# Performance work log

Hardware: AMD Instinct MI355X
Metric: run time of the kernel (lower is better)

The kernel has to match this reference:

```python
import jax, jax.numpy as jnp
import numpy as np

DN = ('NCHW', 'OIHW', 'NCHW')

def _conv(x, W, pad):
    return jax.lax.conv_general_dilated(x, W, (1, 1), [(pad, pad), (pad, pad)], dimension_numbers=DN)

def _cbs(x, W, s, b, pad):
    # Conv2d(bias=False) + folded BatchNorm (scale/bias) + SiLU
    y = _conv(x, W, pad) * s[None, :, None, None] + b[None, :, None, None]
    return y * jax.nn.sigmoid(y)

def _l2norm(x):
    n = jnp.sqrt(jnp.sum(x * x, axis=1, keepdims=True))
    return x / jnp.maximum(n, 1e-12)

def setup_inputs() -> dict:
    key = jax.random.key(0)
    ks = jax.random.split(key, 24)
    B, C, H, L, TD, NC = 16, 256, 64, 40, 768, 8
    EMB = (TD + NC * 2) // 2  # 392
    w = lambda k, sh: jax.random.normal(k, sh, jnp.float32) * 0.02
    img = jax.random.normal(ks[0], (B, C, H, H), jnp.float32)
    flang = jax.random.normal(ks[1], (B, L, TD), jnp.float32)
    lengths = jax.random.randint(ks[2], (B, 1), 5, L + 1)
    word_mask = (jnp.arange(L)[None, :] < lengths).astype(jnp.int32)
    return {
        'img': img, 'flang': flang, 'word_mask': word_mask, 'sigma_w': 0.1,
        'W1': w(ks[3], (EMB, TD)), 'b1': w(ks[4], (EMB,)),
        'W2': w(ks[5], (NC * 2, EMB)), 'b2': w(ks[6], (NC * 2,)),
        'Wv': w(ks[7], (C, C, 1, 1)), 'sv': jnp.ones((C,)), 'bv': w(ks[8], (C,)),
        'Wg': w(ks[9], (NC, NC, 1, 1)), 'sg': jnp.ones((NC,)), 'bg': w(ks[10], (NC,)),
        'Wb': w(ks[11], (NC, NC, 1, 1)), 'sb': jnp.ones((NC,)), 'bb': w(ks[12], (NC,)),
        'Wf1': w(ks[13], (C, C, 1, 1)), 'sf1': jnp.ones((C,)), 'bf1': w(ks[14], (C,)),
        'Wf2': w(ks[15], (C, C, 3, 3)), 'sf2': jnp.ones((C,)), 'bf2': w(ks[16], (C,)),
        'Wf3': w(ks[17], (C, C, 1, 1)), 'bf3': w(ks[18], (C,)),
        'Ws': w(ks[19], (NC, C, 3, 3)), 'bs': w(ks[20], (NC,)),
        'add_weight': jnp.zeros((), jnp.float32),
    }

def reference(img, flang, word_mask, sigma_w, W1, b1, W2, b2, Wv, sv, bv,
              Wg, sg, bg, Wb, sb, bb, Wf1, sf1, bf1, Wf2, sf2, bf2,
              Wf3, bf3, Ws, bs, add_weight):
    B, C, H = img.shape[0], img.shape[1], img.shape[2]
    nc = Wg.shape[0]
    map_visu = jnp.tanh(_cbs(img, Wv, sv, bv, 0))
    # ragged masked mean excluding first (CLS) and last (SEP) masked tokens
    m = word_mask.astype(jnp.float32)
    c = jnp.cumsum(m, axis=1)
    tot = c[:, -1:]
    inc = m * ((c > 1) & (c < tot)).astype(jnp.float32)  # [B,L]
    flang_avg = jnp.sum(flang * inc[:, :, None], axis=1) / jnp.sum(inc, axis=1, keepdims=True)
    map_flang = jax.nn.sigmoid((flang_avg @ W1.T + b1) @ W2.T + b2)  # [B,2*nc]
    maps = map_flang.reshape(B, nc, 2)
    sigma_x = sigma_w * H
    sig = _conv(img, Ws, 0) + bs[None, :, None, None]  # [B,nc,H-2,H-2]
    sigma_weight = jax.nn.sigmoid(jnp.mean(sig, axis=(2, 3), keepdims=True))  # [B,nc,1,1]
    sigma_y = sigma_x * sigma_weight
    yc = (maps[:, :, 0] * H).astype(jnp.int32).astype(jnp.float32)[:, :, None, None]
    xc = (maps[:, :, 1] * H).astype(jnp.int32).astype(jnp.float32)[:, :, None, None]
    gy = jnp.arange(H, dtype=jnp.float32)[None, None, :, None]
    gx = jnp.arange(H, dtype=jnp.float32)[None, None, None, :]
    weights = jnp.exp(-((gy - yc) ** 2 / (2.0 * sigma_y ** 2) + (gx - xc) ** 2 / (2.0 * sigma_x ** 2)))  # [B,nc,H,H]
    gamma = jnp.tanh(_cbs(weights, Wg, sg, bg, 0))
    beta = jnp.tanh(_cbs(weights, Wb, sb, bb, 0))
    g = jnp.mean(gamma, axis=1, keepdims=True)
    bmax = jnp.max(beta, axis=1, keepdims=True)
    v_film = _l2norm(g * map_visu + bmax)
    v_film = _cbs(v_film, Wf1, sf1, bf1, 0)
    v_film = _cbs(v_film, Wf2, sf2, bf2, 1)
    v_film = _conv(v_film, Wf3, 0) + bf3[None, :, None, None]
    aw = jnp.tanh(add_weight)
    v_add = (1.0 + aw) * img + (1.0 - aw) * v_film
    return _l2norm(v_add)
```

## Files before the change

kernel.cpp:

```cpp
#include <hip/hip_runtime.h>
#include <hip/hip_bf16.h>


#define DEVFN static __device__ __forceinline__

DEVFN float sigmoidf_(float x) { return 1.f / (1.f + expf(-x)); }
DEVFN float siluf_(float y) { return y / (1.f + expf(-y)); }

typedef __attribute__((ext_vector_type(8))) short bf16x8;
typedef __attribute__((ext_vector_type(4))) float f32x4;

DEVFN unsigned short f2bf_(float f) {
    union { __hip_bfloat16 b; unsigned short u; } cv;
    cv.b = __float2bfloat16(f);
    return cv.u;
}

__global__ void prep_kernel(const float* __restrict__ Wv, const float* __restrict__ Wf1,
                            const float* __restrict__ Wf3, const float* __restrict__ Wf2,
                            short* __restrict__ WvB, short* __restrict__ W1B,
                            short* __restrict__ W3B, short* __restrict__ WB2) {
    int idx = blockIdx.x * 256 + threadIdx.x;
    if (idx < 65536) {
        int j    = idx & 7;
        int lane = (idx >> 3) & 63;
        int coT  = (idx >> 9) & 15;
        int ci32 = (idx >> 13) & 7;
        int co = coT * 16 + (lane & 15);
        int ci = ci32 * 32 + ((lane >> 4) << 3) + j;
        int src = co * 256 + ci;
        WvB[idx] = (short)f2bf_(Wv[src]);
        W1B[idx] = (short)f2bf_(Wf1[src]);
        W3B[idx] = (short)f2bf_(Wf3[src]);
    }
    int o = idx - 65536;
    if (o >= 0 && o < 589824) {
        int j    = o & 7;
        int lane = (o >> 3) & 63;
        int coT  = (o >> 9) & 15;
        int ci32 = (o >> 13) & 7;
        int kk   = o >> 16;
        int co = coT * 16 + (lane & 15);
        int ci = ci32 * 32 + ((lane >> 4) << 3) + j;
        WB2[o] = (short)f2bf_(Wf2[(co * 256 + ci) * 9 + kk]);
    }
}

__global__ void lang_kernel(const float* __restrict__ flang, const int* __restrict__ mask,
                            float* __restrict__ fa) {
    __shared__ float inc[40];
    __shared__ float isum;
    int b = blockIdx.x, t = threadIdx.x;
    if (t == 0) {
        float cum[40];
        float c = 0.f;
        for (int l = 0; l < 40; ++l) { c += (float)mask[b * 40 + l]; cum[l] = c; }
        float tot = c, s = 0.f;
        for (int l = 0; l < 40; ++l) {
            float m = (float)mask[b * 40 + l];
            float v = (cum[l] > 1.f && cum[l] < tot) ? m : 0.f;
            inc[l] = v; s += v;
        }
        isum = s;
    }
    __syncthreads();
    for (int d = t; d < 768; d += 256) {
        float a = 0.f;
        for (int l = 0; l < 40; ++l) a += flang[(size_t)(b * 40 + l) * 768 + d] * inc[l];
        fa[b * 768 + d] = a / isum;
    }
}

__global__ void mlp_kernel(const float* __restrict__ fa_g, const float* __restrict__ W1,
                           const float* __restrict__ b1, const float* __restrict__ W2,
                           const float* __restrict__ b2, float* __restrict__ ycxc) {
    __shared__ float fa[768];
    __shared__ float h[392];
    __shared__ float o[16];
    int b = blockIdx.x, t = threadIdx.x;
    for (int k = t; k < 768; k += 448) fa[k] = fa_g[b * 768 + k];
    __syncthreads();
    if (t < 392) {
        float a = b1[t];
        const float* w = W1 + (size_t)t * 768;
        for (int k = 0; k < 768; ++k) a = fmaf(fa[k], w[k], a);
        h[t] = a;
    }
    __syncthreads();
    if (t < 16) {
        float a = b2[t];
        const float* w = W2 + (size_t)t * 392;
        for (int k = 0; k < 392; ++k) a = fmaf(h[k], w[k], a);
        o[t] = sigmoidf_(a);
    }
    __syncthreads();
    if (t < 8) {
        ycxc[b * 8 + t]       = (float)(int)(o[2 * t] * 64.f);
        ycxc[128 + b * 8 + t] = (float)(int)(o[2 * t + 1] * 64.f);
    }
}

__global__ void wsum_kernel(const float* __restrict__ img, float* __restrict__ S) {
    __shared__ float red[9 * 256];
    int bc = blockIdx.x;
    int t = threadIdx.x;
    float s[9];
#pragma unroll
    for (int k = 0; k < 9; ++k) s[k] = 0.f;
    const float* p = img + (size_t)bc * 4096;
    for (int j = 0; j < 16; ++j) {
        int idx = t + j * 256;
        int y = idx >> 6, x = idx & 63;
        float v = p[idx];
#pragma unroll
        for (int ky = 0; ky < 3; ++ky) {
            if (y < ky || y > ky + 61) continue;
#pragma unroll
            for (int kx = 0; kx < 3; ++kx) {
                if (x < kx || x > kx + 61) continue;
                s[ky * 3 + kx] += v;
            }
        }
    }
#pragma unroll
    for (int k = 0; k < 9; ++k) red[k * 256 + t] = s[k];
    __syncthreads();
    for (int st = 128; st > 0; st >>= 1) {
        if (t < st) {
#pragma unroll
            for (int k = 0; k < 9; ++k) red[k * 256 + t] += red[k * 256 + t + st];
        }
        __syncthreads();
    }
    if (t < 9) S[(size_t)bc * 9 + t] = red[t * 256];
}

__global__ void sigw_kernel(const float* __restrict__ Ws, const float* __restrict__ S,
                            const float* __restrict__ bs, float* __restrict__ sigw) {
    __shared__ float red[8 * 256];
    int b = blockIdx.x, t = threadIdx.x;
    float sv[9];
    const float* Sp = S + (size_t)(b * 256 + t) * 9;
#pragma unroll
    for (int k = 0; k < 9; ++k) sv[k] = Sp[k];
#pragma unroll
    for (int co = 0; co < 8; ++co) {
        const float* wp = Ws + (size_t)(co * 256 + t) * 9;
        float a = 0.f;
#pragma unroll
        for (int k = 0; k < 9; ++k) a = fmaf(wp[k], sv[k], a);
        red[co * 256 + t] = a;
    }
    __syncthreads();
    for (int st = 128; st > 0; st >>= 1) {
        if (t < st) {
#pragma unroll
            for (int co = 0; co < 8; ++co) red[co * 256 + t] += red[co * 256 + t + st];
        }
        __syncthreads();
    }
    if (t < 8) sigw[b * 8 + t] = sigmoidf_(red[t * 256] / 3844.f + bs[t]);
}

__global__ void gauss_kernel(const float* __restrict__ ycxc, const float* __restrict__ sigw,
                             const float* __restrict__ sigma_w,
                             const float* __restrict__ Wg, const float* __restrict__ sg,
                             const float* __restrict__ bg,
                             const float* __restrict__ Wb, const float* __restrict__ sb,
                             const float* __restrict__ bb,
                             float* __restrict__ g, float* __restrict__ bm) {
    int blk = blockIdx.x;
    int b = blk >> 6, y = blk & 63;
    int x = threadIdx.x;
    float sx = sigma_w[0] * 64.f;
    float w[8];
#pragma unroll
    for (int n = 0; n < 8; ++n) {
        float yc = ycxc[b * 8 + n], xc = ycxc[128 + b * 8 + n];
        float sy = sx * sigw[b * 8 + n];
        float dy = (float)y - yc, dx = (float)x - xc;
        w[n] = expf(-(dy * dy / (2.f * sy * sy) + dx * dx / (2.f * sx * sx)));
    }
    float gacc = 0.f, bmax = -3.4e38f;
#pragma unroll
    for (int n = 0; n < 8; ++n) {
        float a1 = 0.f, a2 = 0.f;
#pragma unroll
        for (int m = 0; m < 8; ++m) {
            a1 = fmaf(Wg[n * 8 + m], w[m], a1);
            a2 = fmaf(Wb[n * 8 + m], w[m], a2);
        }
        float ga = tanhf(siluf_(a1 * sg[n] + bg[n]));
        float be = tanhf(siluf_(a2 * sb[n] + bb[n]));
        gacc += ga;
        bmax = fmaxf(bmax, be);
    }
    g[(size_t)(b * 64 + y) * 64 + x] = gacc * 0.125f;
    bm[(size_t)(b * 64 + y) * 64 + x] = bmax;
}

template <int MODE>
__global__ __launch_bounds__(256) void mfma1x1(
        const float* __restrict__ inF,
        const __hip_bfloat16* __restrict__ inB,
        const short* __restrict__ wb,
        const float* __restrict__ sc, const float* __restrict__ bi,
        const float* __restrict__ g, const float* __restrict__ bm,
        const float* __restrict__ img, const float* __restrict__ addw,
        __hip_bfloat16* __restrict__ outB, float* __restrict__ outF) {
    __shared__ __attribute__((aligned(16))) short lA[64 * 264];
    __shared__ float ls_s[256], ls_b[256];
    __shared__ float ls_g[64], ls_bm[64];
    int blk = blockIdx.x, b = blk >> 6, y = blk & 63;
    int t = threadIdx.x, w = t >> 6, lane = t & 63;
    int lx = lane & 15, koct = lane >> 4;

    if (MODE != 2) { ls_s[t] = sc[t]; }
    ls_b[t] = bi[t];
    if (MODE == 0 && t < 64) {
        ls_g[t]  = g[(size_t)(b * 64 + y) * 64 + t];
        ls_bm[t] = bm[(size_t)(b * 64 + y) * 64 + t];
    }

    if (MODE == 0) {
        int x = t & 63, cg = t >> 6;
        const float* ib = inF + (size_t)b * 1048576 + y * 64 + x;
#pragma unroll
        for (int c8 = 0; c8 < 8; ++c8) {
            int ci0 = cg * 64 + c8 * 8;
            unsigned short r[8];
#pragma unroll
            for (int j = 0; j < 8; ++j) r[j] = f2bf_(ib[(size_t)(ci0 + j) * 4096]);
            *(uint4*)&lA[x * 264 + ci0] = *(uint4*)r;
        }
    } else {
        const unsigned short* xg = (const unsigned short*)inB + (size_t)(b * 64 + y) * 16384;
#pragma unroll
        for (int it = 0; it < 8; ++it) {
            int e8 = t + it * 256;
            int x2 = e8 >> 5, c8 = e8 & 31;
            *(uint4*)&lA[x2 * 264 + c8 * 8] = *(const uint4*)(xg + e8 * 8);
        }
    }

    f32x4 acc[4][4];
#pragma unroll
    for (int mi = 0; mi < 4; ++mi)
#pragma unroll
        for (int ni = 0; ni < 4; ++ni) acc[mi][ni] = (f32x4){0.f, 0.f, 0.f, 0.f};
    __syncthreads();

#pragma unroll
    for (int k32 = 0; k32 < 8; ++k32) {
        const short* wp = wb + (((k32 * 16) + w * 4) * 64 + lane) * 8;
        bf16x8 bfr[4];
#pragma unroll
        for (int ni = 0; ni < 4; ++ni) bfr[ni] = *(const bf16x8*)(wp + ni * 512);
        bf16x8 afr[4];
#pragma unroll
        for (int mi = 0; mi < 4; ++mi)
            afr[mi] = *(const bf16x8*)&lA[(mi * 16 + lx) * 264 + k32 * 32 + koct * 8];
#pragma unroll
        for (int mi = 0; mi < 4; ++mi)
#pragma unroll
            for (int ni = 0; ni < 4; ++ni)
                acc[mi][ni] = __builtin_amdgcn_mfma_f32_16x16x32_bf16(afr[mi], bfr[ni], acc[mi][ni], 0, 0, 0);
    }

    if constexpr (MODE == 0) {
        __shared__ float pr[4096];
        __shared__ float invs[64];
#pragma unroll
        for (int mi = 0; mi < 4; ++mi)
#pragma unroll
            for (int rr = 0; rr < 4; ++rr) {
                int x = mi * 16 + koct * 4 + rr;
                float ps = 0.f;
#pragma unroll
                for (int ni = 0; ni < 4; ++ni) {
                    int co = w * 64 + ni * 16 + lx;
                    float yv = fmaf(acc[mi][ni][rr], ls_s[co], ls_b[co]);
                    float mvv = tanhf(siluf_(yv));
                    float v = fmaf(ls_g[x], mvv, ls_bm[x]);
                    acc[mi][ni][rr] = v;
                    ps += v * v;
                }
                pr[x * 64 + w * 16 + lx] = ps;
            }
        __syncthreads();
        if (t < 64) {
            float s2 = 0.f;
            for (int q = 0; q < 64; ++q) s2 += pr[t * 64 + q];
            invs[t] = 1.f / fmaxf(sqrtf(s2), 1e-12f);
        }
        __syncthreads();
#pragma unroll
        for (int mi = 0; mi < 4; ++mi)
#pragma unroll
            for (int ni = 0; ni < 4; ++ni) {
                int co = w * 64 + ni * 16 + lx;
#pragma unroll
                for (int rr = 0; rr < 4; ++rr) {
                    int x = mi * 16 + koct * 4 + rr;
                    lA[x * 264 + co] = (short)f2bf_(acc[mi][ni][rr] * invs[x]);
                }
            }
        __syncthreads();
        unsigned short* og = (unsigned short*)outB + (size_t)(b * 64 + y) * 16384;
#pragma unroll
        for (int it = 0; it < 8; ++it) {
            int e8 = t + it * 256;
            int x2 = e8 >> 5, c8 = e8 & 31;
            *(uint4*)(og + e8 * 8) = *(uint4*)&lA[x2 * 264 + c8 * 8];
        }
    } else if constexpr (MODE == 1) {
        __syncthreads();
#pragma unroll
        for (int mi = 0; mi < 4; ++mi)
#pragma unroll
            for (int ni = 0; ni < 4; ++ni) {
                int co = w * 64 + ni * 16 + lx;
#pragma unroll
                for (int rr = 0; rr < 4; ++rr) {
                    int x = mi * 16 + koct * 4 + rr;
                    float yv = fmaf(acc[mi][ni][rr], ls_s[co], ls_b[co]);
                    lA[x * 264 + co] = (short)f2bf_(siluf_(yv));
                }
            }
        __syncthreads();
        unsigned short* og = (unsigned short*)outB + (size_t)(b * 64 + y) * 16384;
#pragma unroll
        for (int it = 0; it < 8; ++it) {
            int e8 = t + it * 256;
            int x2 = e8 >> 5, c8 = e8 & 31;
            *(uint4*)(og + e8 * 8) = *(uint4*)&lA[x2 * 264 + c8 * 8];
        }
    } else {
        __shared__ float pr[4096];
        __shared__ float invs[64];
        float aw = tanhf(addw[0]);
#pragma unroll
        for (int mi = 0; mi < 4; ++mi)
#pragma unroll
            for (int ni = 0; ni < 4; ++ni) {
                int co = w * 64 + ni * 16 + lx;
                const float* ip = img + ((size_t)(b * 256 + co) * 64 + y) * 64 + mi * 16 + koct * 4;
                float4 im = *(const float4*)ip;
                float imv[4] = {im.x, im.y, im.z, im.w};
#pragma unroll
                for (int rr = 0; rr < 4; ++rr) {
                    float v = (1.f + aw) * imv[rr] + (1.f - aw) * (acc[mi][ni][rr] + ls_b[co]);
                    acc[mi][ni][rr] = v;
                }
            }
#pragma unroll
        for (int mi = 0; mi < 4; ++mi)
#pragma unroll
            for (int rr = 0; rr < 4; ++rr) {
                int x = mi * 16 + koct * 4 + rr;
                float ps = 0.f;
#pragma unroll
                for (int ni = 0; ni < 4; ++ni) ps += acc[mi][ni][rr] * acc[mi][ni][rr];
                pr[x * 64 + w * 16 + lx] = ps;
            }
        __syncthreads();
        if (t < 64) {
            float s2 = 0.f;
            for (int q = 0; q < 64; ++q) s2 += pr[t * 64 + q];
            invs[t] = 1.f / fmaxf(sqrtf(s2), 1e-12f);
        }
        __syncthreads();
#pragma unroll
        for (int mi = 0; mi < 4; ++mi)
#pragma unroll
            for (int ni = 0; ni < 4; ++ni) {
                int co = w * 64 + ni * 16 + lx;
                float r[4];
#pragma unroll
                for (int rr = 0; rr < 4; ++rr) {
                    int x = mi * 16 + koct * 4 + rr;
                    r[rr] = acc[mi][ni][rr] * invs[x];
                }
                float* op = outF + ((size_t)(b * 256 + co) * 64 + y) * 64 + mi * 16 + koct * 4;
                *(float4*)op = *(float4*)r;
            }
    }
}

__global__ __launch_bounds__(256, 3) void conv3x3_mfma(const __hip_bfloat16* __restrict__ xin,
                                                       const short* __restrict__ wb,
                                                       const float* __restrict__ sc,
                                                       const float* __restrict__ bi,
                                                       __hip_bfloat16* __restrict__ outB) {
    __shared__ __attribute__((aligned(16))) short lds[64 * 264];
    int blk = blockIdx.x;
    int b = blk >> 6, y = blk & 63;
    int t = threadIdx.x;
    int w = t >> 6, lane = t & 63;
    int lx = lane & 15, koct = lane >> 4;
    const unsigned short* xg = (const unsigned short*)xin + (size_t)b * 1048576;

    f32x4 acc[4][4];
#pragma unroll
    for (int mi = 0; mi < 4; ++mi)
#pragma unroll
        for (int ni = 0; ni < 4; ++ni) acc[mi][ni] = (f32x4){0.f, 0.f, 0.f, 0.f};

    for (int cc = 0; cc < 4; ++cc) {
        __syncthreads();
#pragma unroll
        for (int p = 0; p < 7; ++p) {
            int u = t + p * 256;
            if (u < 1584) {
                int r = u / 528;
                int rem = u - r * 528;
                int xp = rem >> 3, ci8 = rem & 7;
                int ys = y + r - 1, xs = xp - 1;
                uint4 v = {0u, 0u, 0u, 0u};
                if (ys >= 0 && ys < 64 && xs >= 0 && xs < 64)
                    v = *(const uint4*)(xg + ((size_t)(ys * 64 + xs) * 256 + cc * 64 + ci8 * 8));
                *(uint4*)&lds[(r * 66 + xp) * 72 + ci8 * 8] = v;
            }
        }
        __syncthreads();
        for (int kk = 0; kk < 9; ++kk) {
            int ky = kk / 3, kx = kk - ky * 3;
#pragma unroll
            for (int k32 = 0; k32 < 2; ++k32) {
                int ci32g = cc * 2 + k32;
                const short* wp = wb + ((((kk * 8 + ci32g) * 16) + w * 4) * 64 + lane) * 8;
                bf16x8 bfr[4];
#pragma unroll
                for (int ni = 0; ni < 4; ++ni)
                    bfr[ni] = *(const bf16x8*)(wp + ni * 512);
                bf16x8 afr[4];
#pragma unroll
                for (int mi = 0; mi < 4; ++mi)
                    afr[mi] = *(const bf16x8*)&lds[(ky * 66 + mi * 16 + lx + kx) * 72 + k32 * 32 + koct * 8];
#pragma unroll
                for (int mi = 0; mi < 4; ++mi)
#pragma unroll
                    for (int ni = 0; ni < 4; ++ni)
                        acc[mi][ni] = __builtin_amdgcn_mfma_f32_16x16x32_bf16(afr[mi], bfr[ni], acc[mi][ni], 0, 0, 0);
            }
        }
    }
    __syncthreads();
#pragma unroll
    for (int ni = 0; ni < 4; ++ni) {
        int co = w * 64 + ni * 16 + lx;
        float s = sc[co], bb2 = bi[co];
#pragma unroll
        for (int mi = 0; mi < 4; ++mi)
#pragma unroll
            for (int rr = 0; rr < 4; ++rr) {
                int x = mi * 16 + koct * 4 + rr;
                float yv = fmaf(acc[mi][ni][rr], s, bb2);
                lds[x * 264 + co] = (short)f2bf_(siluf_(yv));
            }
    }
    __syncthreads();
    unsigned short* og = (unsigned short*)outB + (size_t)(b * 64 + y) * 16384;
#pragma unroll
    for (int it = 0; it < 8; ++it) {
        int e8 = t + it * 256;
        int x2 = e8 >> 5, c8 = e8 & 31;
        *(uint4*)(og + e8 * 8) = *(uint4*)&lds[x2 * 264 + c8 * 8];
    }
}

extern "C" void kernel_launch(void* const* d_in, const int* in_sizes, int n_in,
                              void* d_out, int out_size, void* d_ws, size_t ws_size,
                              hipStream_t stream) {
    const float* img     = (const float*)d_in[0];
    const float* flang   = (const float*)d_in[1];
    const int*   wmask   = (const int*)d_in[2];
    const float* sigma_w = (const float*)d_in[3];
    const float* W1      = (const float*)d_in[4];
    const float* b1      = (const float*)d_in[5];
    const float* W2      = (const float*)d_in[6];
    const float* b2      = (const float*)d_in[7];
    const float* Wv      = (const float*)d_in[8];
    const float* sv      = (const float*)d_in[9];
    const float* bv      = (const float*)d_in[10];
    const float* Wg      = (const float*)d_in[11];
    const float* sg      = (const float*)d_in[12];
    const float* bg      = (const float*)d_in[13];
    const float* Wb      = (const float*)d_in[14];
    const float* sb      = (const float*)d_in[15];
    const float* bb      = (const float*)d_in[16];
    const float* Wf1     = (const float*)d_in[17];
    const float* sf1     = (const float*)d_in[18];
    const float* bf1     = (const float*)d_in[19];
    const float* Wf2     = (const float*)d_in[20];
    const float* sf2     = (const float*)d_in[21];
    const float* bf2     = (const float*)d_in[22];
    const float* Wf3     = (const float*)d_in[23];
    const float* bf3     = (const float*)d_in[24];
    const float* Ws      = (const float*)d_in[25];
    const float* bs      = (const float*)d_in[26];
    const float* addw    = (const float*)d_in[27];
    float* out = (float*)d_out;
    float* ws  = (float*)d_ws;

    short* WvB  = (short*)ws;
    short* W1B  = (short*)(ws + 32768);
    short* W3B  = (short*)(ws + 65536);
    short* WB2  = (short*)(ws + 98304);
    float* fa   = ws + 393216;
    float* ycxc = ws + 405504;
    float* S    = ws + 405760;
    float* sigw = ws + 442624;
    float* gmap = ws + 442752;
    float* bmap = ws + 508288;
    __hip_bfloat16* bufA = (__hip_bfloat16*)(ws + 573824);
    __hip_bfloat16* bufB = (__hip_bfloat16*)(ws + 8962432);

    prep_kernel<<<2560, 256, 0, stream>>>(Wv, Wf1, Wf3, Wf2, WvB, W1B, W3B, WB2);
    lang_kernel<<<16, 256, 0, stream>>>(flang, wmask, fa);
    mlp_kernel<<<16, 448, 0, stream>>>(fa, W1, b1, W2, b2, ycxc);
    wsum_kernel<<<4096, 256, 0, stream>>>(img, S);
    sigw_kernel<<<16, 256, 0, stream>>>(Ws, S, bs, sigw);
    gauss_kernel<<<1024, 64, 0, stream>>>(ycxc, sigw, sigma_w, Wg, sg, bg, Wb, sb, bb, gmap, bmap);
    mfma1x1<0><<<1024, 256, 0, stream>>>(img, nullptr, WvB, sv, bv, gmap, bmap,
                                         nullptr, nullptr, bufA, nullptr);
    mfma1x1<1><<<1024, 256, 0, stream>>>(nullptr, bufA, W1B, sf1, bf1, nullptr, nullptr,
                                         nullptr, nullptr, bufB, nullptr);
    conv3x3_mfma<<<1024, 256, 0, stream>>>(bufB, WB2, sf2, bf2, bufA);
    mfma1x1<2><<<1024, 256, 0, stream>>>(nullptr, bufA, W3B, nullptr, bf3, nullptr, nullptr,
                                         img, addw, nullptr, out);
}
```

Before: 465.7 us.

## Fuse Wv and Wf1 1x1 convs; process two rows per 3x3 conv block

Merges the first two 1x1 MFMA convolutions into one kernel, so the normalized FiLM activations stay in LDS and are never written to or re-read from global memory. The 3x3 conv now computes two output rows per block with a 4-row halo tile. This reuses the halo loads and weight fragments across both rows, at the cost of doubling accumulator registers (occupancy hint lowered to 2). The final 1x1 conv is split into its own kernel, and the pr scratch array is aliased onto LDS to reduce shared memory use.

```diff
diff --git a/kernel.cpp b/kernel.cpp
--- a/kernel.cpp
+++ b/kernel.cpp
@@ -199,32 +199,32 @@
     bm[(size_t)(b * 64 + y) * 64 + x] = bmax;
 }
 
-template <int MODE>
-__global__ __launch_bounds__(256) void mfma1x1(
-        const float* __restrict__ inF,
-        const __hip_bfloat16* __restrict__ inB,
-        const short* __restrict__ wb,
-        const float* __restrict__ sc, const float* __restrict__ bi,
+__global__ __launch_bounds__(256) void f01_kernel(
+        const float* __restrict__ img, const short* __restrict__ wvb,
+        const short* __restrict__ w1b,
+        const float* __restrict__ sv, const float* __restrict__ bv,
+        const float* __restrict__ s1, const float* __restrict__ b1,
         const float* __restrict__ g, const float* __restrict__ bm,
-        const float* __restrict__ img, const float* __restrict__ addw,
-        __hip_bfloat16* __restrict__ outB, float* __restrict__ outF) {
+        __hip_bfloat16* __restrict__ outB) {
     __shared__ __attribute__((aligned(16))) short lA[64 * 264];
-    __shared__ float ls_s[256], ls_b[256];
+    __shared__ float invs[64];
+    __shared__ float ls_sv[256], ls_bv[256], ls_s1[256], ls_b1[256];
     __shared__ float ls_g[64], ls_bm[64];
+    float* pr = (float*)lA;
     int blk = blockIdx.x, b = blk >> 6, y = blk & 63;
     int t = threadIdx.x, w = t >> 6, lane = t & 63;
     int lx = lane & 15, koct = lane >> 4;
 
-    if (MODE != 2) { ls_s[t] = sc[t]; }
-    ls_b[t] = bi[t];
-    if (MODE == 0 && t < 64) {
+    ls_sv[t] = sv[t]; ls_bv[t] = bv[t];
+    ls_s1[t] = s1[t]; ls_b1[t] = b1[t];
+    if (t < 64) {
         ls_g[t]  = g[(size_t)(b * 64 + y) * 64 + t];
         ls_bm[t] = bm[(size_t)(b * 64 + y) * 64 + t];
     }
 
-    if (MODE == 0) {
+    {
         int x = t & 63, cg = t >> 6;
-        const float* ib = inF + (size_t)b * 1048576 + y * 64 + x;
+        const float* ib = img + (size_t)b * 1048576 + y * 64 + x;
 #pragma unroll
         for (int c8 = 0; c8 < 8; ++c8) {
             int ci0 = cg * 64 + c8 * 8;
@@ -233,16 +233,7 @@
             for (int j = 0; j < 8; ++j) r[j] = f2bf_(ib[(size_t)(ci0 + j) * 4096]);
             *(uint4*)&lA[x * 264 + ci0] = *(uint4*)r;
         }
-    } else {
-        const unsigned short* xg = (const unsigned short*)inB + (size_t)(b * 64 + y) * 16384;
-#pragma unroll
-        for (int it = 0; it < 8; ++it) {
-            int e8 = t + it * 256;
-            int x2 = e8 >> 5, c8 = e8 & 31;
-            *(uint4*)&lA[x2 * 264 + c8 * 8] = *(const uint4*)(xg + e8 * 8);
-        }
-    }
-
+    }
     f32x4 acc[4][4];
 #pragma unroll
     for (int mi = 0; mi < 4; ++mi)
@@ -252,7 +243,7 @@
 
 #pragma unroll
     for (int k32 = 0; k32 < 8; ++k32) {
-        const short* wp = wb + (((k32 * 16) + w * 4) * 64 + lane) * 8;
+        const short* wp = wvb + (((k32 * 16) + w * 4) * 64 + lane) * 8;
         bf16x8 bfr[4];
 #pragma unroll
         for (int ni = 0; ni < 4; ++ni) bfr[ni] = *(const bf16x8*)(wp + ni * 512);
@@ -266,156 +257,119 @@
             for (int ni = 0; ni < 4; ++ni)
                 acc[mi][ni] = __builtin_amdgcn_mfma_f32_16x16x32_bf16(afr[mi], bfr[ni], acc[mi][ni], 0, 0, 0);
     }
-
-    if constexpr (MODE == 0) {
-        __shared__ float pr[4096];
-        __shared__ float invs[64];
-#pragma unroll
-        for (int mi = 0; mi < 4; ++mi)
+    __syncthreads();
+
+#pragma unroll
+    for (int mi = 0; mi < 4; ++mi)
+#pragma unroll
+        for (int rr = 0; rr < 4; ++rr) {
+            int x = mi * 16 + koct * 4 + rr;
+            float ps = 0.f;
+#pragma unroll
+            for (int ni = 0; ni < 4; ++ni) {
+                int co = w * 64 + ni * 16 + lx;
+                float yv = fmaf(acc[mi][ni][rr], ls_sv[co], ls_bv[co]);
+                float mvv = tanhf(siluf_(yv));
+                float v = fmaf(ls_g[x], mvv, ls_bm[x]);
+                acc[mi][ni][rr] = v;
+                ps += v * v;
+            }
+            pr[x * 64 + w * 16 + lx] = ps;
+        }
+    __syncthreads();
+    if (t < 64) {
+        float s2 = 0.f;
+        for (int q = 0; q < 64; ++q) s2 += pr[t * 64 + q];
+        invs[t] = 1.f / fmaxf(sqrtf(s2), 1e-12f);
+    }
+    __syncthreads();
+
+#pragma unroll
+    for (int mi = 0; mi < 4; ++mi)
+#pragma unroll
+        for (int ni = 0; ni < 4; ++ni) {
+            int co = w * 64 + ni * 16 + lx;
 #pragma unroll
             for (int rr = 0; rr < 4; ++rr) {
                 int x = mi * 16 + koct * 4 + rr;
-                float ps = 0.f;
-#pragma unroll
-                for (int ni = 0; ni < 4; ++ni) {
-                    int co = w * 64 + ni * 16 + lx;
-                    float yv = fmaf(acc[mi][ni][rr], ls_s[co], ls_b[co]);
-                    float mvv = tanhf(siluf_(yv));
-                    float v = fmaf(ls_g[x], mvv, ls_bm[x]);
-                    acc[mi][ni][rr] = v;
-                    ps += v * v;
-                }
-                pr[x * 64 + w * 16 + lx] = ps;
-            }
-        __syncthreads();
-        if (t < 64) {
-            float s2 = 0.f;
-            for (int q = 0; q < 64; ++q) s2 += pr[t * 64 + q];
-            invs[t] = 1.f / fmaxf(sqrtf(s2), 1e-12f);
-        }
-        __syncthreads();
+                lA[x * 264 + co] = (short)f2bf_(acc[mi][ni][rr] * invs[x]);
+            }
+        }
+#pragma unroll
+    for (int mi = 0; mi < 4; ++mi)
+#pragma unroll
+        for (int ni = 0; ni < 4; ++ni) acc[mi][ni] = (f32x4){0.f, 0.f, 0.f, 0.f};
+    __syncthreads();
+
+#pragma unroll
+    for (int k32 = 0; k32 < 8; ++k32) {
+        const short* wp = w1b + (((k32 * 16) + w * 4) * 64 + lane) * 8;
+        bf16x8 bfr[4];
+#pragma unroll
+        for (int ni = 0; ni < 4; ++ni) bfr[ni] = *(const bf16x8*)(wp + ni * 512);
+        bf16x8 afr[4];
 #pragma unroll
         for (int mi = 0; mi < 4; ++mi)
-#pragma unroll
-            for (int ni = 0; ni < 4; ++ni) {
-                int co = w * 64 + ni * 16 + lx;
-#pragma unroll
-                for (int rr = 0; rr < 4; ++rr) {
-                    int x = mi * 16 + koct * 4 + rr;
-                    lA[x * 264 + co] = (short)f2bf_(acc[mi][ni][rr] * invs[x]);
-                }
-            }
-        __syncthreads();
-        unsigned short* og = (unsigned short*)outB + (size_t)(b * 64 + y) * 16384;
-#pragma unroll
-        for (int it = 0; it < 8; ++it) {
-            int e8 = t + it * 256;
-            int x2 = e8 >> 5, c8 = e8 & 31;
-            *(uint4*)(og + e8 * 8) = *(uint4*)&lA[x2 * 264 + c8 * 8];
-        }
-    } else if constexpr (MODE == 1) {
-        __syncthreads();
+            afr[mi] = *(const bf16x8*)&lA[(mi * 16 + lx) * 264 + k32 * 32 + koct * 8];
 #pragma unroll
         for (int mi = 0; mi < 4; ++mi)
 #pragma unroll
-            for (int ni = 0; ni < 4; ++ni) {
-                int co = w * 64 + ni * 16 + lx;
-#pragma unroll
-                for (int rr = 0; rr < 4; ++rr) {
-                    int x = mi * 16 + koct * 4 + rr;
-                    float yv = fmaf(acc[mi][ni][rr], ls_s[co], ls_b[co]);
-                    lA[x * 264 + co] = (short)f2bf_(siluf_(yv));
-                }
-            }
-        __syncthreads();
-        unsigned short* og = (unsigned short*)outB + (size_t)(b * 64 + y) * 16384;
-#pragma unroll
-        for (int it = 0; it < 8; ++it) {
-            int e8 = t + it * 256;
-            int x2 = e8 >> 5, c8 = e8 & 31;
-            *(uint4*)(og + e8 * 8) = *(uint4*)&lA[x2 * 264 + c8 * 8];
-        }
-    } else {
-        __shared__ float pr[4096];
-        __shared__ float invs[64];
-        float aw = tanhf(addw[0]);
-#pragma unroll
-        for (int mi = 0; mi < 4; ++mi)
-#pragma unroll
-            for (int ni = 0; ni < 4; ++ni) {
-                int co = w * 64 + ni * 16 + lx;
-                const float* ip = img + ((size_t)(b * 256 + co) * 64 + y) * 64 + mi * 16 + koct * 4;
-                float4 im = *(const float4*)ip;
-                float imv[4] = {im.x, im.y, im.z, im.w};
-#pragma unroll
-                for (int rr = 0; rr < 4; ++rr) {
-                    float v = (1.f + aw) * imv[rr] + (1.f - aw) * (acc[mi][ni][rr] + ls_b[co]);
-                    acc[mi][ni][rr] = v;
-                }
-            }
-#pragma unroll
-        for (int mi = 0; mi < 4; ++mi)
+            for (int ni = 0; ni < 4; ++ni)
+                acc[mi][ni] = __builtin_amdgcn_mfma_f32_16x16x32_bf16(afr[mi], bfr[ni], acc[mi][ni], 0, 0, 0);
+    }
+    __syncthreads();
+
+#pragma unroll
+    for (int mi = 0; mi < 4; ++mi)
+#pragma unroll
+        for (int ni = 0; ni < 4; ++ni) {
+            int co = w * 64 + ni * 16 + lx;
 #pragma unroll
             for (int rr = 0; rr < 4; ++rr) {
                 int x = mi * 16 + koct * 4 + rr;
-                float ps = 0.f;
-#pragma unroll
-                for (int ni = 0; ni < 4; ++ni) ps += acc[mi][ni][rr] * acc[mi][ni][rr];
-                pr[x * 64 + w * 16 + lx] = ps;
-            }
-        __syncthreads();
-        if (t < 64) {
-            float s2 = 0.f;
-            for (int q = 0; q < 64; ++q) s2 += pr[t * 64 + q];
-            invs[t] = 1.f / fmaxf(sqrtf(s2), 1e-12f);
-        }
-        __syncthreads();
-#pragma unroll
-        for (int mi = 0; mi < 4; ++mi)
-#pragma unroll
-            for (int ni = 0; ni < 4; ++ni) {
-                int co = w * 64 + ni * 16 + lx;
-                float r[4];
-#pragma unroll
-                for (int rr = 0; rr < 4; ++rr) {
-                    int x = mi * 16 + koct * 4 + rr;
-                    r[rr] = acc[mi][ni][rr] * invs[x];
-                }
-                float* op = outF + ((size_t)(b * 256 + co) * 64 + y) * 64 + mi * 16 + koct * 4;
-                *(float4*)op = *(float4*)r;
-            }
-    }
-}
-
-__global__ __launch_bounds__(256, 3) void conv3x3_mfma(const __hip_bfloat16* __restrict__ xin,
+                float yv = fmaf(acc[mi][ni][rr], ls_s1[co], ls_b1[co]);
+                lA[x * 264 + co] = (short)f2bf_(siluf_(yv));
+            }
+        }
+    __syncthreads();
+    unsigned short* og = (unsigned short*)outB + (size_t)(b * 64 + y) * 16384;
+#pragma unroll
+    for (int it = 0; it < 8; ++it) {
+        int e8 = t + it * 256;
+        int x2 = e8 >> 5, c8 = e8 & 31;
+        *(uint4*)(og + e8 * 8) = *(uint4*)&lA[x2 * 264 + c8 * 8];
+    }
+}
+
+__global__ __launch_bounds__(256, 2) void conv3x3_mfma(const __hip_bfloat16* __restrict__ xin,
                                                        const short* __restrict__ wb,
                                                        const float* __restrict__ sc,
                                                        const float* __restrict__ bi,
                                                        __hip_bfloat16* __restrict__ outB) {
-    __shared__ __attribute__((aligned(16))) short lds[64 * 264];
+    __shared__ __attribute__((aligned(16))) short lds[4 * 66 * 72];
     int blk = blockIdx.x;
-    int b = blk >> 6, y = blk & 63;
+    int b = blk >> 5, y0 = (blk & 31) * 2;
     int t = threadIdx.x;
     int w = t >> 6, lane = t & 63;
     int lx = lane & 15, koct = lane >> 4;
     const unsigned short* xg = (const unsigned short*)xin + (size_t)b * 1048576;
 
-    f32x4 acc[4][4];
-#pragma unroll
-    for (int mi = 0; mi < 4; ++mi)
+    f32x4 acc[8][4];
+#pragma unroll
+    for (int mi = 0; mi < 8; ++mi)
 #pragma unroll
         for (int ni = 0; ni < 4; ++ni) acc[mi][ni] = (f32x4){0.f, 0.f, 0.f, 0.f};
 
     for (int cc = 0; cc < 4; ++cc) {
         __syncthreads();
 #pragma unroll
-        for (int p = 0; p < 7; ++p) {
+        for (int p = 0; p < 9; ++p) {
             int u = t + p * 256;
-            if (u < 1584) {
+            if (u < 2112) {
                 int r = u / 528;
                 int rem = u - r * 528;
                 int xp = rem >> 3, ci8 = rem & 7;
-                int ys = y + r - 1, xs = xp - 1;
+                int ys = y0 + r - 1, xs = xp - 1;
                 uint4 v = {0u, 0u, 0u, 0u};
                 if (ys >= 0 && ys < 64 && xs >= 0 && xs < 64)
                     v = *(const uint4*)(xg + ((size_t)(ys * 64 + xs) * 256 + cc * 64 + ci8 * 8));
@@ -433,40 +387,142 @@
 #pragma unroll
                 for (int ni = 0; ni < 4; ++ni)
                     bfr[ni] = *(const bf16x8*)(wp + ni * 512);
-                bf16x8 afr[4];
-#pragma unroll
-                for (int mi = 0; mi < 4; ++mi)
-                    afr[mi] = *(const bf16x8*)&lds[(ky * 66 + mi * 16 + lx + kx) * 72 + k32 * 32 + koct * 8];
-#pragma unroll
-                for (int mi = 0; mi < 4; ++mi)
+                bf16x8 afr[8];
+#pragma unroll
+                for (int mi = 0; mi < 8; ++mi) {
+                    int row = mi >> 2, xb = (mi & 3) * 16;
+                    afr[mi] = *(const bf16x8*)&lds[((row + ky) * 66 + xb + lx + kx) * 72 + k32 * 32 + koct * 8];
+                }
+#pragma unroll
+                for (int mi = 0; mi < 8; ++mi)
 #pragma unroll
                     for (int ni = 0; ni < 4; ++ni)
                         acc[mi][ni] = __builtin_amdgcn_mfma_f32_16x16x32_bf16(afr[mi], bfr[ni], acc[mi][ni], 0, 0, 0);
             }
         }
     }
-    __syncthreads();
-#pragma unroll
-    for (int ni = 0; ni < 4; ++ni) {
-        int co = w * 64 + ni * 16 + lx;
-        float s = sc[co], bb2 = bi[co];
-#pragma unroll
-        for (int mi = 0; mi < 4; ++mi)
-#pragma unroll
-            for (int rr = 0; rr < 4; ++rr) {
-                int x = mi * 16 + koct * 4 + rr;
-                float yv = fmaf(acc[mi][ni][rr], s, bb2);
-                lds[x * 264 + co] = (short)f2bf_(siluf_(yv));
-            }
-    }
-    __syncthreads();
-    unsigned short* og = (unsigned short*)outB + (size_t)(b * 64 + y) * 16384;
+#pragma unroll
+    for (int r2 = 0; r2 < 2; ++r2) {
+        __syncthreads();
+#pragma unroll
+        for (int mi4 = 0; mi4 < 4; ++mi4) {
+            int mi = r2 * 4 + mi4;
+#pragma unroll
+            for (int ni = 0; ni < 4; ++ni) {
+                int co = w * 64 + ni * 16 + lx;
+                float s = sc[co], bb2 = bi[co];
+#pragma unroll
+                for (int rr = 0; rr < 4; ++rr) {
+                    int x = mi4 * 16 + koct * 4 + rr;
+                    float yv = fmaf(acc[mi][ni][rr], s, bb2);
+                    lds[x * 264 + co] = (short)f2bf_(siluf_(yv));
+                }
+            }
+        }
+        __syncthreads();
+        unsigned short* og = (unsigned short*)outB + (size_t)(b * 64 + y0 + r2) * 16384;
+#pragma unroll
+        for (int it = 0; it < 8; ++it) {
+            int e8 = t + it * 256;
+            int x2 = e8 >> 5, c8 = e8 & 31;
+            *(uint4*)(og + e8 * 8) = *(uint4*)&lds[x2 * 264 + c8 * 8];
+        }
+    }
+}
+
+__global__ __launch_bounds__(256) void final_mfma(const __hip_bfloat16* __restrict__ inB,
+                                                  const short* __restrict__ w3b,
+                                                  const float* __restrict__ bf3,
+                                                  const float* __restrict__ img,
+                                                  const float* __restrict__ addw,
+                                                  float* __restrict__ outF) {
+    __shared__ __attribute__((aligned(16))) short lA[64 * 264];
+    __shared__ float invs[64];
+    __shared__ float ls_b[256];
+    float* pr = (float*)lA;
+    int blk = blockIdx.x, b = blk >> 6, y = blk & 63;
+    int t = threadIdx.x, w = t >> 6, lane = t & 63;
+    int lx = lane & 15, koct = lane >> 4;
+    ls_b[t] = bf3[t];
+
+    const unsigned short* xg = (const unsigned short*)inB + (size_t)(b * 64 + y) * 16384;
 #pragma unroll
     for (int it = 0; it < 8; ++it) {
         int e8 = t + it * 256;
         int x2 = e8 >> 5, c8 = e8 & 31;
-        *(uint4*)(og + e8 * 8) = *(uint4*)&lds[x2 * 264 + c8 * 8];
-    }
+        *(uint4*)&lA[x2 * 264 + c8 * 8] = *(const uint4*)(xg + e8 * 8);
+    }
+    f32x4 acc[4][4];
+#pragma unroll
+    for (int mi = 0; mi < 4; ++mi)
+#pragma unroll
+        for (int ni = 0; ni < 4; ++ni) acc[mi][ni] = (f32x4){0.f, 0.f, 0.f, 0.f};
+    __syncthreads();
+
+#pragma unroll
+    for (int k32 = 0; k32 < 8; ++k32) {
+        const short* wp = w3b + (((k32 * 16) + w * 4) * 64 + lane) * 8;
+        bf16x8 bfr[4];
+#pragma unroll
+        for (int ni = 0; ni < 4; ++ni) bfr[ni] = *(const bf16x8*)(wp + ni * 512);
+        bf16x8 afr[4];
+#pragma unroll
+        for (int mi = 0; mi < 4; ++mi)
+            afr[mi] = *(const bf16x8*)&lA[(mi * 16 + lx) * 264 + k32 * 32 + koct * 8];
+#pragma unroll
+        for (int mi = 0; mi < 4; ++mi)
+#pragma unroll
+            for (int ni = 0; ni < 4; ++ni)
+                acc[mi][ni] = __builtin_amdgcn_mfma_f32_16x16x32_bf16(afr[mi], bfr[ni], acc[mi][ni], 0, 0, 0);
+    }
+    __syncthreads();
+
+    float aw = tanhf(addw[0]);
+#pragma unroll
+    for (int mi = 0; mi < 4; ++mi)
+#pragma unroll
+        for (int ni = 0; ni < 4; ++ni) {
+            int co = w * 64 + ni * 16 + lx;
+            const float* ip = img + ((size_t)(b * 256 + co) * 64 + y) * 64 + mi * 16 + koct * 4;
+            float4 im = *(const float4*)ip;
+            float imv[4] = {im.x, im.y, im.z, im.w};
+#pragma unroll
+            for (int rr = 0; rr < 4; ++rr) {
+                float v = (1.f + aw) * imv[rr] + (1.f - aw) * (acc[mi][ni][rr] + ls_b[co]);
+                acc[mi][ni][rr] = v;
+            }
+        }
+#pragma unroll
+    for (int mi = 0; mi < 4; ++mi)
+#pragma unroll
+        for (int rr = 0; rr < 4; ++rr) {
+            int x = mi * 16 + koct * 4 + rr;
+            float ps = 0.f;
+#pragma unroll
+            for (int ni = 0; ni < 4; ++ni) ps += acc[mi][ni][rr] * acc[mi][ni][rr];
+            pr[x * 64 + w * 16 + lx] = ps;
+        }
+    __syncthreads();
+    if (t < 64) {
+        float s2 = 0.f;
+        for (int q = 0; q < 64; ++q) s2 += pr[t * 64 + q];
+        invs[t] = 1.f / fmaxf(sqrtf(s2), 1e-12f);
+    }
+    __syncthreads();
+#pragma unroll
+    for (int mi = 0; mi < 4; ++mi)
+#pragma unroll
+        for (int ni = 0; ni < 4; ++ni) {
+            int co = w * 64 + ni * 16 + lx;
+            float r[4];
+#pragma unroll
+            for (int rr = 0; rr < 4; ++rr) {
+                int x = mi * 16 + koct * 4 + rr;
+                r[rr] = acc[mi][ni][rr] * invs[x];
+            }
+            float* op = outF + ((size_t)(b * 256 + co) * 64 + y) * 64 + mi * 16 + koct * 4;
+            *(float4*)op = *(float4*)r;
+        }
 }
 
 extern "C" void kernel_launch(void* const* d_in, const int* in_sizes, int n_in,
@@ -522,11 +578,7 @@
     wsum_kernel<<<4096, 256, 0, stream>>>(img, S);
     sigw_kernel<<<16, 256, 0, stream>>>(Ws, S, bs, sigw);
     gauss_kernel<<<1024, 64, 0, stream>>>(ycxc, sigw, sigma_w, Wg, sg, bg, Wb, sb, bb, gmap, bmap);
-    mfma1x1<0><<<1024, 256, 0, stream>>>(img, nullptr, WvB, sv, bv, gmap, bmap,
-                                         nullptr, nullptr, bufA, nullptr);
-    mfma1x1<1><<<1024, 256, 0, stream>>>(nullptr, bufA, W1B, sf1, bf1, nullptr, nullptr,
-                                         nullptr, nullptr, bufB, nullptr);
-    conv3x3_mfma<<<1024, 256, 0, stream>>>(bufB, WB2, sf2, bf2, bufA);
-    mfma1x1<2><<<1024, 256, 0, stream>>>(nullptr, bufA, W3B, nullptr, bf3, nullptr, nullptr,
-                                         img, addw, nullptr, out);
-}
+    f01_kernel<<<1024, 256, 0, stream>>>(img, WvB, W1B, sv, bv, sf1, bf1, gmap, bmap, bufB);
+    conv3x3_mfma<<<512, 256, 0, stream>>>(bufB, WB2, sf2, bf2, bufA);
+    final_mfma<<<1024, 256, 0, stream>>>(bufA, W3B, bf3, img, addw, out);
+}
```

Result: faster. 430.0 us (-7.7%).
